# Kernel optimization log

Measured on AMD Instinct MI355X. Metric: run time of the kernel, lower is better.

## Reference

```python
import jax, jax.numpy as jnp
import numpy as np

N = 100000   # nodes
E = 1600000  # edges
R = 4        # relations (bond types)
D_IN = 38    # atom feature dim
H = 64       # hidden dim
G = 1000     # graphs in batch
O = 1        # output tasks


def layer_norm(h, g, b):
    mu = h.mean(-1, keepdims=True)
    var = ((h - mu) ** 2).mean(-1, keepdims=True)
    return (h - mu) / jnp.sqrt(var + 1e-5) * g + b


def rgcn_conv(x, src, dst, etype, W, root_w, bias):
    # PyG RGCNConv with aggr='mean': per-relation mean of neighbor features,
    # then per-relation linear transform (mean commutes with the linear map),
    # plus root transform and bias.
    msg = x[src]                                   # [E, F] gather (memory-bound)
    seg = dst * R + etype                          # fused (node, relation) segment id
    sums = jax.ops.segment_sum(msg, seg, num_segments=N * R)          # [N*R, F]
    cnt = jax.ops.segment_sum(jnp.ones((msg.shape[0],), x.dtype), seg,
                              num_segments=N * R)                     # [N*R]
    mean = sums / jnp.maximum(cnt, 1.0)[:, None]
    mean = mean.reshape(N, R, x.shape[-1])         # [N, R, F]
    return jnp.einsum('nri,rio->no', mean, W) + x @ root_w + bias


def setup_inputs() -> dict:
    key = jax.random.key(0)
    ks = jax.random.split(key, 32)
    s = lambda k, sh: (jax.random.normal(k, sh, jnp.float32) * 0.05)
    inp = {
        'x': jax.random.normal(ks[0], (N, D_IN), jnp.float32),
        'edge_index': jax.random.randint(ks[1], (2, E), 0, N),
        'edge_type': jax.random.randint(ks[2], (E,), 0, R),
        'batch': jnp.sort(jax.random.randint(ks[3], (N,), 0, G)),
        # layer 0 (D_IN -> H), with linear residual projection
        'W0': s(ks[4], (R, D_IN, H)), 'root0': s(ks[5], (D_IN, H)), 'b0': jnp.zeros((H,), jnp.float32),
        'ln0_g': jnp.ones((H,), jnp.float32), 'ln0_b': jnp.zeros((H,), jnp.float32),
        'res_w': s(ks[6], (D_IN, H)), 'res_b': jnp.zeros((H,), jnp.float32),
        # layer 1
        'W1': s(ks[7], (R, H, H)), 'root1': s(ks[8], (H, H)), 'b1': jnp.zeros((H,), jnp.float32),
        'ln1_g': jnp.ones((H,), jnp.float32), 'ln1_b': jnp.zeros((H,), jnp.float32),
        # layer 2
        'W2': s(ks[9], (R, H, H)), 'root2': s(ks[10], (H, H)), 'b2': jnp.zeros((H,), jnp.float32),
        'ln2_g': jnp.ones((H,), jnp.float32), 'ln2_b': jnp.zeros((H,), jnp.float32),
        # readout MLP
        'ro_w1': s(ks[11], (H, H)), 'ro_b1': jnp.zeros((H,), jnp.float32),
        'ro_w2': s(ks[12], (H, O)), 'ro_b2': jnp.zeros((O,), jnp.float32),
    }
    return inp


def reference(x, edge_index, edge_type, batch,
              W0, root0, b0, ln0_g, ln0_b, res_w, res_b,
              W1, root1, b1, ln1_g, ln1_b,
              W2, root2, b2, ln2_g, ln2_b,
              ro_w1, ro_b1, ro_w2, ro_b2):
    src, dst = edge_index[0], edge_index[1]
    # dropout is inference-mode (identity)
    h = jax.nn.relu(rgcn_conv(x, src, dst, edge_type, W0, root0, b0))
    x1 = layer_norm(h + x @ res_w + res_b, ln0_g, ln0_b)
    h = jax.nn.relu(rgcn_conv(x1, src, dst, edge_type, W1, root1, b1))
    x2 = layer_norm(h + x1, ln1_g, ln1_b)
    h = jax.nn.relu(rgcn_conv(x2, src, dst, edge_type, W2, root2, b2))
    x3 = layer_norm(h + x2, ln2_g, ln2_b)
    # global mean pool over graphs
    pooled = jax.ops.segment_sum(x3, batch, num_segments=G)
    cnt = jax.ops.segment_sum(jnp.ones((N,), x3.dtype), batch, num_segments=G)
    pooled = pooled / jnp.maximum(cnt, 1.0)[:, None]
    out = jax.nn.relu(pooled @ ro_w1 + ro_b1) @ ro_w2 + ro_b2  # [G, O]
    return out
```

## Files before the change

### kernel.cpp

```cpp
#include <hip/hip_runtime.h>
#include <math.h>

#define NNODES 100000
#define NEDGES 1600000
#define NREL   4
#define DIN    38
#define HID    64
#define NGRAPH 1000
#define NSEG   (NNODES * NREL)
#define NSCANB ((NSEG + 1023) / 1024)
#define YW     320

__device__ __forceinline__ float wsum64(float v) {
    #pragma unroll
    for (int o = 32; o; o >>= 1) v += __shfl_xor(v, o);
    return v;
}

__device__ __forceinline__ void ln_group_reduce(float& s) {
    s += __shfl_xor(s, 1);
    s += __shfl_xor(s, 2);
    s += __shfl_xor(s, 4);
    s += __shfl_xor(s, 8);
}

__global__ __launch_bounds__(256) void count_kernel(
    const int* __restrict__ ei, const int* __restrict__ et,
    const int* __restrict__ batch, int* __restrict__ cnt,
    int* __restrict__ gcnt) {
    int i = blockIdx.x * 256 + threadIdx.x;
    if (i < NEDGES) {
        int dst = ei[NEDGES + i];
        atomicAdd(&cnt[dst * NREL + et[i]], 1);
    }
    if (i < NNODES) {
        atomicAdd(&gcnt[batch[i]], 1);
    }
}

__global__ __launch_bounds__(256) void scan1_kernel(
    const int* __restrict__ cnt, int* __restrict__ excl, int* __restrict__ bsum) {
    __shared__ int tmp[256];
    int tid = threadIdx.x;
    int base = blockIdx.x * 1024 + tid * 4;
    int v0 = 0, v1 = 0, v2 = 0, v3 = 0;
    if (base + 0 < NSEG) v0 = cnt[base + 0];
    if (base + 1 < NSEG) v1 = cnt[base + 1];
    if (base + 2 < NSEG) v2 = cnt[base + 2];
    if (base + 3 < NSEG) v3 = cnt[base + 3];
    int s = v0 + v1 + v2 + v3;
    tmp[tid] = s;
    __syncthreads();
    for (int off = 1; off < 256; off <<= 1) {
        int t = (tid >= off) ? tmp[tid - off] : 0;
        __syncthreads();
        tmp[tid] += t;
        __syncthreads();
    }
    if (tid == 255) bsum[blockIdx.x] = tmp[255];
    int run = tmp[tid] - s;
    if (base + 0 < NSEG) excl[base + 0] = run; run += v0;
    if (base + 1 < NSEG) excl[base + 1] = run; run += v1;
    if (base + 2 < NSEG) excl[base + 2] = run; run += v2;
    if (base + 3 < NSEG) excl[base + 3] = run;
}

__global__ __launch_bounds__(512) void scan2_kernel(int* __restrict__ bsum) {
    __shared__ int tmp[512];
    int tid = threadIdx.x;
    int v = (tid < NSCANB) ? bsum[tid] : 0;
    tmp[tid] = v;
    __syncthreads();
    for (int off = 1; off < 512; off <<= 1) {
        int t = (tid >= off) ? tmp[tid - off] : 0;
        __syncthreads();
        tmp[tid] += t;
        __syncthreads();
    }
    if (tid < NSCANB) bsum[tid] = tmp[tid] - v;
}

__global__ __launch_bounds__(256) void place_kernel(
    const int* __restrict__ ei, const int* __restrict__ et,
    const int* __restrict__ excl, const int* __restrict__ bsum,
    int* __restrict__ fill, int* __restrict__ esrc) {
    int e = blockIdx.x * 256 + threadIdx.x;
    if (e >= NEDGES) return;
    int r = et[e];
    int seg = ei[NEDGES + e] * NREL + r;
    int pos = excl[seg] + bsum[seg >> 10] + atomicAdd(&fill[seg], 1);
    esrc[pos] = ei[e] | (r << 20);
}

__global__ __launch_bounds__(256, 4) void gemm12_kernel(
    const float* __restrict__ x, const float* __restrict__ W,
    const float* __restrict__ root, float* __restrict__ y) {
    __shared__ float As[64][68];
    __shared__ float Ws[64][68];
    int tid = threadIdx.x;
    int nbase = blockIdx.x * 64;

    {
        int sk = tid & 63, sm0 = tid >> 6;
        #pragma unroll
        for (int mm = 0; mm < 16; ++mm) {
            int m = sm0 + mm * 4;
            int n = nbase + m; if (n > NNODES - 1) n = NNODES - 1;
            As[sk][m] = x[(size_t)n * 64 + sk];
        }
    }
    int r = tid >> 4, c = tid & 15;
    int scc = tid & 63, sk0 = tid >> 6;

    for (int nc = 0; nc < 5; ++nc) {
        __syncthreads();
        const float* src = (nc < 4) ? (W + nc * 4096) : root;
        #pragma unroll
        for (int kk = 0; kk < 16; ++kk) {
            int k = sk0 + kk * 4;
            Ws[k][scc] = src[k * 64 + scc];
        }
        __syncthreads();
        float acc[4][4] = {};
        #pragma unroll 4
        for (int k = 0; k < 64; ++k) {
            const float4 av = *(const float4*)&As[k][r * 4];
            const float4 wv = *(const float4*)&Ws[k][c * 4];
            const float a_[4] = {av.x, av.y, av.z, av.w};
            const float w_[4] = {wv.x, wv.y, wv.z, wv.w};
            #pragma unroll
            for (int i = 0; i < 4; ++i)
                #pragma unroll
                for (int j = 0; j < 4; ++j)
                    acc[i][j] += a_[i] * w_[j];
        }
        #pragma unroll
        for (int i = 0; i < 4; ++i) {
            int n = nbase + r * 4 + i;
            if (n < NNODES)
                *(float4*)&y[(size_t)n * YW + nc * 64 + c * 4] =
                    make_float4(acc[i][0], acc[i][1], acc[i][2], acc[i][3]);
        }
    }
}

__global__ __launch_bounds__(256, 4) void gemm0_kernel(
    const float* __restrict__ x, const float* __restrict__ W0,
    const float* __restrict__ root0, const float* __restrict__ resw,
    float* __restrict__ y, float* __restrict__ xres) {
    __shared__ float As[38][68];
    __shared__ float Ws[38][68];
    int tid = threadIdx.x;
    int nbase = blockIdx.x * 64;

    for (int idx = tid; idx < 64 * 38; idx += 256) {
        int m = idx / 38, k = idx - m * 38;
        int n = nbase + m; if (n > NNODES - 1) n = NNODES - 1;
        As[k][m] = x[(size_t)n * DIN + k];
    }
    int r = tid >> 4, c = tid & 15;

    for (int nc = 0; nc < 6; ++nc) {
        __syncthreads();
        const float* src = (nc < 4) ? (W0 + nc * DIN * 64)
                                    : (nc == 4 ? root0 : resw);
        for (int idx = tid; idx < 38 * 64; idx += 256) {
            int k = idx >> 6, cc = idx & 63;
            Ws[k][cc] = src[idx];
        }
        __syncthreads();
        float acc[4][4] = {};
        #pragma unroll 2
        for (int k = 0; k < 38; ++k) {
            const float4 av = *(const float4*)&As[k][r * 4];
            const float4 wv = *(const float4*)&Ws[k][c * 4];
            const float a_[4] = {av.x, av.y, av.z, av.w};
            const float w_[4] = {wv.x, wv.y, wv.z, wv.w};
            #pragma unroll
            for (int i = 0; i < 4; ++i)
                #pragma unroll
                for (int j = 0; j < 4; ++j)
                    acc[i][j] += a_[i] * w_[j];
        }
        #pragma unroll
        for (int i = 0; i < 4; ++i) {
            int n = nbase + r * 4 + i;
            if (n < NNODES) {
                float4 o = make_float4(acc[i][0], acc[i][1], acc[i][2], acc[i][3]);
                if (nc < 5) *(float4*)&y[(size_t)n * YW + nc * 64 + c * 4] = o;
                else        *(float4*)&xres[(size_t)n * 64 + c * 4] = o;
            }
        }
    }
}

template <bool L0, bool POOL>
__global__ __launch_bounds__(256, 8) void epi_kernel(
    const float* __restrict__ y, const float* __restrict__ xprev,
    const int* __restrict__ esrc, const int* __restrict__ excl,
    const int* __restrict__ bsum, const int* __restrict__ cnt,
    const float* __restrict__ bias, const float* __restrict__ bias2,
    const float* __restrict__ lng, const float* __restrict__ lnb,
    const int* __restrict__ batch, float* __restrict__ dst) {
    int n = (blockIdx.x * 256 + threadIdx.x) >> 6;
    int lane = threadIdx.x & 63;
    if (n >= NNODES) return;
    int q = lane >> 4;
    int cl = lane & 15;

    int s4 = n * 4;
    int myc = 0, myb = 0;
    if (lane < 4) {
        myc = cnt[s4 + lane];
        myb = excl[s4 + lane] + bsum[(s4 + lane) >> 10];
    }
    float myi = 1.f / fmaxf((float)myc, 1.f);
    int c0 = __shfl(myc, 0), c1 = __shfl(myc, 1);
    int c2 = __shfl(myc, 2), c3 = __shfl(myc, 3);
    float i0 = __shfl(myi, 0), i1 = __shfl(myi, 1);
    float i2 = __shfl(myi, 2), i3 = __shfl(myi, 3);
    int beg = __shfl(myb, 0);
    int ctot = c0 + c1 + c2 + c3;

    float acc[4] = {0.f, 0.f, 0.f, 0.f};
    for (int base = 0; base < ctot; base += 64) {
        int rem = ctot - base; if (rem > 64) rem = 64;
        int raw = (lane < rem) ? esrc[beg + base + lane] : 0;
        int src = raw & 0xFFFFF;
        int rel = raw >> 20;
        int moff = src * 5 + rel;
        float ic = (rel & 2) ? ((rel & 1) ? i3 : i2)
                             : ((rel & 1) ? i1 : i0);
        if (lane >= rem) ic = 0.f;

        int it = (rem + 3) >> 2;
        int i = 0;
        for (; i + 4 <= it; i += 4) {
            int l0 = (i + 0) * 4 + q, l1 = (i + 1) * 4 + q;
            int l2 = (i + 2) * 4 + q, l3 = (i + 3) * 4 + q;
            int o0 = __shfl(moff, l0), o1 = __shfl(moff, l1);
            int o2 = __shfl(moff, l2), o3 = __shfl(moff, l3);
            float s0 = __shfl(ic, l0), s1 = __shfl(ic, l1);
            float s2 = __shfl(ic, l2), s3 = __shfl(ic, l3);
            const float4 v0 = *(const float4*)&y[(size_t)o0 * 64 + cl * 4];
            const float4 v1 = *(const float4*)&y[(size_t)o1 * 64 + cl * 4];
            const float4 v2 = *(const float4*)&y[(size_t)o2 * 64 + cl * 4];
            const float4 v3 = *(const float4*)&y[(size_t)o3 * 64 + cl * 4];
            acc[0] += v0.x * s0; acc[1] += v0.y * s0;
            acc[2] += v0.z * s0; acc[3] += v0.w * s0;
            acc[0] += v1.x * s1; acc[1] += v1.y * s1;
            acc[2] += v1.z * s1; acc[3] += v1.w * s1;
            acc[0] += v2.x * s2; acc[1] += v2.y * s2;
            acc[2] += v2.z * s2; acc[3] += v2.w * s2;
            acc[0] += v3.x * s3; acc[1] += v3.y * s3;
            acc[2] += v3.z * s3; acc[3] += v3.w * s3;
        }
        for (; i < it; ++i) {
            int l = i * 4 + q;
            int o = __shfl(moff, l);
            float sc = __shfl(ic, l);
            const float4 v = *(const float4*)&y[(size_t)o * 64 + cl * 4];
            acc[0] += v.x * sc; acc[1] += v.y * sc;
            acc[2] += v.z * sc; acc[3] += v.w * sc;
        }
    }
    #pragma unroll
    for (int j = 0; j < 4; ++j) {
        acc[j] += __shfl_xor(acc[j], 16);
        acc[j] += __shfl_xor(acc[j], 32);
    }

    const float4 yr = *(const float4*)&y[(size_t)n * YW + 256 + cl * 4];
    const float4 bv = *(const float4*)&bias[cl * 4];
    const float4 rv = *(const float4*)&xprev[(size_t)n * 64 + cl * 4];
    const float y_[4] = {yr.x, yr.y, yr.z, yr.w};
    const float b_[4] = {bv.x, bv.y, bv.z, bv.w};
    const float r_[4] = {rv.x, rv.y, rv.z, rv.w};
    float u[4];
    float s = 0.f;
    #pragma unroll
    for (int j = 0; j < 4; ++j) {
        u[j] = fmaxf(acc[j] + y_[j] + b_[j], 0.f) + r_[j];
        s += u[j];
    }
    if (L0) {
        const float4 sv = *(const float4*)&bias2[cl * 4];
        const float s2_[4] = {sv.x, sv.y, sv.z, sv.w};
        #pragma unroll
        for (int j = 0; j < 4; ++j) { u[j] += s2_[j]; s += s2_[j]; }
    }
    ln_group_reduce(s);
    float mu = s * (1.f / 64.f);
    float qq = 0.f;
    #pragma unroll
    for (int j = 0; j < 4; ++j) { u[j] -= mu; qq += u[j] * u[j]; }
    ln_group_reduce(qq);
    float inv = 1.f / sqrtf(qq * (1.f / 64.f) + 1e-5f);
    const float4 gv = *(const float4*)&lng[cl * 4];
    const float4 ev = *(const float4*)&lnb[cl * 4];
    const float g_[4] = {gv.x, gv.y, gv.z, gv.w};
    const float e_[4] = {ev.x, ev.y, ev.z, ev.w};
    float oq = u[q] * inv * g_[q] + e_[q];
    if (POOL) {
        int g = batch[n];
        atomicAdd(dst + (size_t)g * 64 + cl * 4 + q, oq);
    } else {
        dst[(size_t)n * 64 + cl * 4 + q] = oq;
    }
}

__global__ __launch_bounds__(256) void readout_kernel(
    const float* __restrict__ pooled, const int* __restrict__ gcnt,
    const float* __restrict__ w1, const float* __restrict__ b1,
    const float* __restrict__ w2, const float* __restrict__ b2,
    float* __restrict__ out) {
    __shared__ float wl[64][64];
    int tid = threadIdx.x;
    for (int idx = tid; idx < 64 * 64; idx += 256) {
        wl[idx >> 6][idx & 63] = w1[idx];
    }
    __syncthreads();
    int wv = tid >> 6, lane = tid & 63;
    int g = blockIdx.x * 4 + wv;
    if (g >= NGRAPH) return;
    int cc = gcnt[g];
    float cf = cc > 0 ? (float)cc : 1.0f;
    float p = pooled[(size_t)g * 64 + lane] / cf;
    float acc = b1[lane];
    for (int f = 0; f < 64; ++f) {
        acc += __shfl(p, f) * wl[f][lane];
    }
    float t = fmaxf(acc, 0.f);
    float v = t * w2[lane];
    v = wsum64(v);
    if (lane == 0) out[g] = v + b2[0];
}

extern "C" void kernel_launch(void* const* d_in, const int* in_sizes, int n_in,
                              void* d_out, int out_size, void* d_ws, size_t ws_size,
                              hipStream_t stream) {
    const float* x     = (const float*)d_in[0];
    const int*   ei    = (const int*)d_in[1];
    const int*   et    = (const int*)d_in[2];
    const int*   batch = (const int*)d_in[3];
    const float* W0    = (const float*)d_in[4];
    const float* root0 = (const float*)d_in[5];
    const float* b0    = (const float*)d_in[6];
    const float* ln0g  = (const float*)d_in[7];
    const float* ln0b  = (const float*)d_in[8];
    const float* resw  = (const float*)d_in[9];
    const float* resb  = (const float*)d_in[10];
    const float* W1    = (const float*)d_in[11];
    const float* root1 = (const float*)d_in[12];
    const float* b1    = (const float*)d_in[13];
    const float* ln1g  = (const float*)d_in[14];
    const float* ln1b  = (const float*)d_in[15];
    const float* W2    = (const float*)d_in[16];
    const float* root2 = (const float*)d_in[17];
    const float* b2    = (const float*)d_in[18];
    const float* ln2g  = (const float*)d_in[19];
    const float* ln2b  = (const float*)d_in[20];
    const float* row1  = (const float*)d_in[21];
    const float* rob1  = (const float*)d_in[22];
    const float* row2  = (const float*)d_in[23];
    const float* rob2  = (const float*)d_in[24];
    float* out = (float*)d_out;

    char* ws = (char*)d_ws;
    size_t off = 0;
    int* cnt    = (int*)(ws + off); off += (size_t)NSEG * 4;
    int* fill   = (int*)(ws + off); off += (size_t)NSEG * 4;
    int* gcnt   = (int*)(ws + off); off += 4096;
    float* pooled = (float*)(ws + off); off += (size_t)NGRAPH * 64 * 4;
    size_t zero_bytes = off;
    int* excl   = (int*)(ws + off); off += (size_t)NSEG * 4;
    int* bsum   = (int*)(ws + off); off += 4096;
    int* esrc   = (int*)(ws + off); off += (size_t)NEDGES * 4;
    float* y    = (float*)(ws + off); off += (size_t)NNODES * YW * 4;
    float* xA   = (float*)(ws + off); off += (size_t)NNODES * 64 * 4;
    float* xB   = (float*)(ws + off); off += (size_t)NNODES * 64 * 4;

    hipMemsetAsync(d_ws, 0, zero_bytes, stream);

    count_kernel<<<6250, 256, 0, stream>>>(ei, et, batch, cnt, gcnt);
    scan1_kernel<<<NSCANB, 256, 0, stream>>>(cnt, excl, bsum);
    scan2_kernel<<<1, 512, 0, stream>>>(bsum);
    place_kernel<<<6250, 256, 0, stream>>>(ei, et, excl, bsum, fill, esrc);

    const int GBLK = (NNODES + 63) / 64;
    const int EBLK = (NNODES + 3) / 4;

    gemm0_kernel<<<GBLK, 256, 0, stream>>>(x, W0, root0, resw, y, xA);
    epi_kernel<true, false><<<EBLK, 256, 0, stream>>>(
        y, xA, esrc, excl, bsum, cnt, b0, resb, ln0g, ln0b, batch, xA);

    gemm12_kernel<<<GBLK, 256, 0, stream>>>(xA, W1, root1, y);
    epi_kernel<false, false><<<EBLK, 256, 0, stream>>>(
        y, xA, esrc, excl, bsum, cnt, b1, resb, ln1g, ln1b, batch, xB);

    gemm12_kernel<<<GBLK, 256, 0, stream>>>(xB, W2, root2, y);
    epi_kernel<false, true><<<EBLK, 256, 0, stream>>>(
        y, xB, esrc, excl, bsum, cnt, b2, resb, ln2g, ln2b, batch, pooled);

    readout_kernel<<<250, 256, 0, stream>>>(
        pooled, gcnt, row1, rob1, row2, rob2, out);
}
```

Measured before the change: 717.1 us.

## Split root output from relation buffer and pool via sorted batch ranges

Stores per-relation transformed features in a dense 256-wide buffer and the root transform in a separate buffer, so gathered message rows align on a 256-float stride. Replaces atomic-based mean pooling and graph counting with a readout that binary-searches the sorted batch array and sums each graph's node rows directly. This removes the atomics and an extra count pass, but requires an additional buffer and relies on batch being sorted.

```diff
diff --git a/kernel.cpp b/kernel.cpp
--- a/kernel.cpp
+++ b/kernel.cpp
@@ -9,7 +9,6 @@
 #define NGRAPH 1000
 #define NSEG   (NNODES * NREL)
 #define NSCANB ((NSEG + 1023) / 1024)
-#define YW     320
 
 __device__ __forceinline__ float wsum64(float v) {
     #pragma unroll
@@ -26,15 +25,11 @@
 
 __global__ __launch_bounds__(256) void count_kernel(
     const int* __restrict__ ei, const int* __restrict__ et,
-    const int* __restrict__ batch, int* __restrict__ cnt,
-    int* __restrict__ gcnt) {
+    int* __restrict__ cnt) {
     int i = blockIdx.x * 256 + threadIdx.x;
     if (i < NEDGES) {
         int dst = ei[NEDGES + i];
         atomicAdd(&cnt[dst * NREL + et[i]], 1);
-    }
-    if (i < NNODES) {
-        atomicAdd(&gcnt[batch[i]], 1);
     }
 }
 
@@ -94,7 +89,8 @@
 
 __global__ __launch_bounds__(256, 4) void gemm12_kernel(
     const float* __restrict__ x, const float* __restrict__ W,
-    const float* __restrict__ root, float* __restrict__ y) {
+    const float* __restrict__ root, float* __restrict__ y,
+    float* __restrict__ yroot) {
     __shared__ float As[64][68];
     __shared__ float Ws[64][68];
     int tid = threadIdx.x;
@@ -137,9 +133,11 @@
         #pragma unroll
         for (int i = 0; i < 4; ++i) {
             int n = nbase + r * 4 + i;
-            if (n < NNODES)
-                *(float4*)&y[(size_t)n * YW + nc * 64 + c * 4] =
-                    make_float4(acc[i][0], acc[i][1], acc[i][2], acc[i][3]);
+            if (n < NNODES) {
+                float4 o = make_float4(acc[i][0], acc[i][1], acc[i][2], acc[i][3]);
+                if (nc < 4) *(float4*)&y[(size_t)n * 256 + nc * 64 + c * 4] = o;
+                else        *(float4*)&yroot[(size_t)n * 64 + c * 4] = o;
+            }
         }
     }
 }
@@ -147,7 +145,7 @@
 __global__ __launch_bounds__(256, 4) void gemm0_kernel(
     const float* __restrict__ x, const float* __restrict__ W0,
     const float* __restrict__ root0, const float* __restrict__ resw,
-    float* __restrict__ y, float* __restrict__ xres) {
+    float* __restrict__ y, float* __restrict__ yroot, float* __restrict__ xres) {
     __shared__ float As[38][68];
     __shared__ float Ws[38][68];
     int tid = threadIdx.x;
@@ -187,21 +185,23 @@
             int n = nbase + r * 4 + i;
             if (n < NNODES) {
                 float4 o = make_float4(acc[i][0], acc[i][1], acc[i][2], acc[i][3]);
-                if (nc < 5) *(float4*)&y[(size_t)n * YW + nc * 64 + c * 4] = o;
-                else        *(float4*)&xres[(size_t)n * 64 + c * 4] = o;
+                if (nc < 4)      *(float4*)&y[(size_t)n * 256 + nc * 64 + c * 4] = o;
+                else if (nc == 4) *(float4*)&yroot[(size_t)n * 64 + c * 4] = o;
+                else             *(float4*)&xres[(size_t)n * 64 + c * 4] = o;
             }
         }
     }
 }
 
-template <bool L0, bool POOL>
+template <bool L0>
 __global__ __launch_bounds__(256, 8) void epi_kernel(
-    const float* __restrict__ y, const float* __restrict__ xprev,
+    const float* __restrict__ y, const float* __restrict__ yroot,
+    const float* __restrict__ xprev,
     const int* __restrict__ esrc, const int* __restrict__ excl,
     const int* __restrict__ bsum, const int* __restrict__ cnt,
     const float* __restrict__ bias, const float* __restrict__ bias2,
     const float* __restrict__ lng, const float* __restrict__ lnb,
-    const int* __restrict__ batch, float* __restrict__ dst) {
+    float* __restrict__ dst) {
     int n = (blockIdx.x * 256 + threadIdx.x) >> 6;
     int lane = threadIdx.x & 63;
     if (n >= NNODES) return;
@@ -228,7 +228,7 @@
         int raw = (lane < rem) ? esrc[beg + base + lane] : 0;
         int src = raw & 0xFFFFF;
         int rel = raw >> 20;
-        int moff = src * 5 + rel;
+        int moff = src * 4 + rel;
         float ic = (rel & 2) ? ((rel & 1) ? i3 : i2)
                              : ((rel & 1) ? i1 : i0);
         if (lane >= rem) ic = 0.f;
@@ -270,7 +270,7 @@
         acc[j] += __shfl_xor(acc[j], 32);
     }
 
-    const float4 yr = *(const float4*)&y[(size_t)n * YW + 256 + cl * 4];
+    const float4 yr = *(const float4*)&yroot[(size_t)n * 64 + cl * 4];
     const float4 bv = *(const float4*)&bias[cl * 4];
     const float4 rv = *(const float4*)&xprev[(size_t)n * 64 + cl * 4];
     const float y_[4] = {yr.x, yr.y, yr.z, yr.w};
@@ -301,16 +301,11 @@
     const float g_[4] = {gv.x, gv.y, gv.z, gv.w};
     const float e_[4] = {ev.x, ev.y, ev.z, ev.w};
     float oq = u[q] * inv * g_[q] + e_[q];
-    if (POOL) {
-        int g = batch[n];
-        atomicAdd(dst + (size_t)g * 64 + cl * 4 + q, oq);
-    } else {
-        dst[(size_t)n * 64 + cl * 4 + q] = oq;
-    }
+    dst[(size_t)n * 64 + cl * 4 + q] = oq;
 }
 
 __global__ __launch_bounds__(256) void readout_kernel(
-    const float* __restrict__ pooled, const int* __restrict__ gcnt,
+    const float* __restrict__ xfin, const int* __restrict__ batch,
     const float* __restrict__ w1, const float* __restrict__ b1,
     const float* __restrict__ w2, const float* __restrict__ b2,
     float* __restrict__ out) {
@@ -323,9 +318,22 @@
     int wv = tid >> 6, lane = tid & 63;
     int g = blockIdx.x * 4 + wv;
     if (g >= NGRAPH) return;
-    int cc = gcnt[g];
-    float cf = cc > 0 ? (float)cc : 1.0f;
-    float p = pooled[(size_t)g * 64 + lane] / cf;
+    int lo = 0, hi = NNODES;
+    while (lo < hi) { int mid = (lo + hi) >> 1; if (batch[mid] < g) lo = mid + 1; else hi = mid; }
+    int lb = lo;
+    hi = NNODES;
+    while (lo < hi) { int mid = (lo + hi) >> 1; if (batch[mid] < g + 1) lo = mid + 1; else hi = mid; }
+    int ub = lo;
+    float s0 = 0.f, s1 = 0.f, s2 = 0.f, s3 = 0.f;
+    int n2 = lb;
+    for (; n2 + 4 <= ub; n2 += 4) {
+        s0 += xfin[(size_t)(n2 + 0) * 64 + lane];
+        s1 += xfin[(size_t)(n2 + 1) * 64 + lane];
+        s2 += xfin[(size_t)(n2 + 2) * 64 + lane];
+        s3 += xfin[(size_t)(n2 + 3) * 64 + lane];
+    }
+    for (; n2 < ub; ++n2) s0 += xfin[(size_t)n2 * 64 + lane];
+    float p = (s0 + s1 + s2 + s3) / fmaxf((float)(ub - lb), 1.f);
     float acc = b1[lane];
     for (int f = 0; f < 64; ++f) {
         acc += __shfl(p, f) * wl[f][lane];
@@ -370,19 +378,18 @@
     size_t off = 0;
     int* cnt    = (int*)(ws + off); off += (size_t)NSEG * 4;
     int* fill   = (int*)(ws + off); off += (size_t)NSEG * 4;
-    int* gcnt   = (int*)(ws + off); off += 4096;
-    float* pooled = (float*)(ws + off); off += (size_t)NGRAPH * 64 * 4;
     size_t zero_bytes = off;
     int* excl   = (int*)(ws + off); off += (size_t)NSEG * 4;
     int* bsum   = (int*)(ws + off); off += 4096;
     int* esrc   = (int*)(ws + off); off += (size_t)NEDGES * 4;
-    float* y    = (float*)(ws + off); off += (size_t)NNODES * YW * 4;
+    float* y    = (float*)(ws + off); off += (size_t)NNODES * 256 * 4;
+    float* yroot= (float*)(ws + off); off += (size_t)NNODES * 64 * 4;
     float* xA   = (float*)(ws + off); off += (size_t)NNODES * 64 * 4;
     float* xB   = (float*)(ws + off); off += (size_t)NNODES * 64 * 4;
 
     hipMemsetAsync(d_ws, 0, zero_bytes, stream);
 
-    count_kernel<<<6250, 256, 0, stream>>>(ei, et, batch, cnt, gcnt);
+    count_kernel<<<6250, 256, 0, stream>>>(ei, et, cnt);
     scan1_kernel<<<NSCANB, 256, 0, stream>>>(cnt, excl, bsum);
     scan2_kernel<<<1, 512, 0, stream>>>(bsum);
     place_kernel<<<6250, 256, 0, stream>>>(ei, et, excl, bsum, fill, esrc);
@@ -390,18 +397,18 @@
     const int GBLK = (NNODES + 63) / 64;
     const int EBLK = (NNODES + 3) / 4;
 
-    gemm0_kernel<<<GBLK, 256, 0, stream>>>(x, W0, root0, resw, y, xA);
-    epi_kernel<true, false><<<EBLK, 256, 0, stream>>>(
-        y, xA, esrc, excl, bsum, cnt, b0, resb, ln0g, ln0b, batch, xA);
-
-    gemm12_kernel<<<GBLK, 256, 0, stream>>>(xA, W1, root1, y);
-    epi_kernel<false, false><<<EBLK, 256, 0, stream>>>(
-        y, xA, esrc, excl, bsum, cnt, b1, resb, ln1g, ln1b, batch, xB);
-
-    gemm12_kernel<<<GBLK, 256, 0, stream>>>(xB, W2, root2, y);
-    epi_kernel<false, true><<<EBLK, 256, 0, stream>>>(
-        y, xB, esrc, excl, bsum, cnt, b2, resb, ln2g, ln2b, batch, pooled);
+    gemm0_kernel<<<GBLK, 256, 0, stream>>>(x, W0, root0, resw, y, yroot, xA);
+    epi_kernel<true><<<EBLK, 256, 0, stream>>>(
+        y, yroot, xA, esrc, excl, bsum, cnt, b0, resb, ln0g, ln0b, xA);
+
+    gemm12_kernel<<<GBLK, 256, 0, stream>>>(xA, W1, root1, y, yroot);
+    epi_kernel<false><<<EBLK, 256, 0, stream>>>(
+        y, yroot, xA, esrc, excl, bsum, cnt, b1, resb, ln1g, ln1b, xB);
+
+    gemm12_kernel<<<GBLK, 256, 0, stream>>>(xB, W2, root2, y, yroot);
+    epi_kernel<false><<<EBLK, 256, 0, stream>>>(
+        y, yroot, xB, esrc, excl, bsum, cnt, b2, resb, ln2g, ln2b, xA);
 
     readout_kernel<<<250, 256, 0, stream>>>(
-        pooled, gcnt, row1, rob1, row2, rob2, out);
-}
+        xA, batch, row1, rob1, row2, rob2, out);
+}
```

Result: faster. 691.9 us (-3.5%).
